# Kernel optimization log

Measured on AMD Instinct MI355X. Metric: run time of the kernel, lower is better.

## Reference

```python
import math
import jax, jax.numpy as jnp
import numpy as np

B, C, H, W = 4, 256, 64, 64
N_HEAD = 4
GROUPS = 32
EPS = 1e-5


def setup_inputs() -> dict:
    key = jax.random.key(0)
    k1, k2, k3 = jax.random.split(key, 3)
    fan = C  # 1x1 conv fan_in
    bound_qkv = math.sqrt(3.0 * 1.0 / ((fan + 3 * C) / 2))
    x = jax.random.normal(k1, (B, C, H, W), dtype=jnp.float32)
    w_qkv = jax.random.uniform(k2, (3 * C, C), dtype=jnp.float32, minval=-bound_qkv, maxval=bound_qkv)
    # out conv has scale=1e-10 init, but use small random weights for a non-trivial baseline
    w_out = jax.random.normal(k3, (C, C), dtype=jnp.float32) * 0.02
    return {
        "x": x,
        "gn_gamma": jnp.ones((C,), jnp.float32),
        "gn_beta": jnp.zeros((C,), jnp.float32),
        "w_qkv": w_qkv,
        "b_qkv": jnp.zeros((3 * C,), jnp.float32),
        "w_out": w_out,
        "b_out": jnp.zeros((C,), jnp.float32),
    }


def _group_norm(x, gamma, beta):
    b, c, h, w = x.shape
    xr = x.reshape(b, GROUPS, c // GROUPS, h, w)
    mean = xr.mean(axis=(2, 3, 4), keepdims=True)
    var = xr.var(axis=(2, 3, 4), keepdims=True)
    xn = ((xr - mean) * jax.lax.rsqrt(var + EPS)).reshape(b, c, h, w)
    return xn * gamma[None, :, None, None] + beta[None, :, None, None]


def reference(x, gn_gamma, gn_beta, w_qkv, b_qkv, w_out, b_out):
    b, c, h, w = x.shape
    head_dim = c // N_HEAD
    norm = _group_norm(x, gn_gamma, gn_beta)
    # 1x1 conv == channel matmul
    qkv = jnp.einsum('oc,bchw->bohw', w_qkv, norm) + b_qkv[None, :, None, None]
    qkv = qkv.reshape(b, N_HEAD, 3 * head_dim, h, w)
    q, k, v = jnp.split(qkv, 3, axis=2)  # each [b, n, d, h, w]
    # note: original scales by sqrt(channel), NOT sqrt(head_dim)
    attn = jnp.einsum('bnchw,bncyx->bnhwyx', q, k) / math.sqrt(c)
    attn = jax.nn.softmax(attn.reshape(b, N_HEAD, h, w, h * w), axis=-1)
    attn = attn.reshape(b, N_HEAD, h, w, h, w)
    out = jnp.einsum('bnhwyx,bncyx->bnchw', attn, v).reshape(b, c, h, w)
    out = jnp.einsum('oc,bchw->bohw', w_out, out) + b_out[None, :, None, None]
    return (out + x) / np.sqrt(2.0).astype(np.float32)
```

## Files before the change

kernel.cpp:

```cpp
#include <hip/hip_runtime.h>
#include <hip/hip_bf16.h>

#define B_   4
#define C_   256
#define HW_  4096
#define GR_  32
#define CPG_ 8
#define EPS_ 1e-5f
#define QSCALE_ 0.09016844005555897f
#define RSQRT2_ 0.70710678118654752f

typedef short bf16x8 __attribute__((ext_vector_type(8)));
typedef short bf16x4 __attribute__((ext_vector_type(4)));
typedef float f32x4  __attribute__((ext_vector_type(4)));
typedef unsigned short u16x4 __attribute__((ext_vector_type(4)));
typedef unsigned int u32x4 __attribute__((ext_vector_type(4)));

__device__ __forceinline__ unsigned short f2bf(float f) {
  unsigned int x; __builtin_memcpy(&x, &f, 4);
  x = x + 0x7FFFu + ((x >> 16) & 1u);
  return (unsigned short)(x >> 16);
}
__device__ __forceinline__ unsigned int cvtpk(float lo, float hi) {
  unsigned int r;
  asm("v_cvt_pk_bf16_f32 %0, %1, %2" : "=v"(r) : "v"(lo), "v"(hi));
  return r;
}
__device__ __forceinline__ float exp2v(float x) {
  float r;
  asm("v_exp_f32 %0, %1" : "=v"(r) : "v"(x));
  return r;
}

#define GP(p) ((const __attribute__((address_space(1))) void*)(p))
#define LP(p) ((__attribute__((address_space(3))) void*)(p))

__global__ __launch_bounds__(256) void wcvt(const float* __restrict__ wqkv,
                                            const float* __restrict__ bqkv,
                                            const float* __restrict__ wout,
                                            unsigned short* __restrict__ wbf,
                                            float* __restrict__ bias_s) {
  int i = blockIdx.x * 256 + threadIdx.x;
  const int NQ = 768 * 256, NO = 256 * 256;
  if (i < NQ) {
    int o = i >> 8;
    float s = ((o % 192) < 64) ? QSCALE_ : 1.0f;
    wbf[i] = f2bf(wqkv[i] * s);
  } else if (i < NQ + NO) {
    wbf[i] = f2bf(wout[i - NQ]);
  } else if (i < NQ + NO + 768) {
    int o = i - NQ - NO;
    float s = ((o % 192) < 64) ? QSCALE_ : 1.0f;
    bias_s[o] = bqkv[o] * s;
  }
}

__global__ __launch_bounds__(256) void gn_stats(const float* __restrict__ x,
                                                float* __restrict__ stats) {
  int bg = blockIdx.x;
  const float4* p = (const float4*)(x + (size_t)bg * (CPG_ * HW_));
  float s = 0.f, ss = 0.f;
  for (int i = threadIdx.x; i < (CPG_ * HW_ / 4); i += 256) {
    float4 v = p[i];
    s  += v.x + v.y + v.z + v.w;
    ss += v.x * v.x + v.y * v.y + v.z * v.z + v.w * v.w;
  }
  #pragma unroll
  for (int off = 32; off > 0; off >>= 1) {
    s  += __shfl_down(s, off, 64);
    ss += __shfl_down(ss, off, 64);
  }
  __shared__ float rs[4], rss[4];
  int wv = threadIdx.x >> 6;
  if ((threadIdx.x & 63) == 0) { rs[wv] = s; rss[wv] = ss; }
  __syncthreads();
  if (threadIdx.x == 0) {
    float S = rs[0] + rs[1] + rs[2] + rs[3];
    float SS = rss[0] + rss[1] + rss[2] + rss[3];
    float mean = S * (1.f / (CPG_ * HW_));
    float var = SS * (1.f / (CPG_ * HW_)) - mean * mean;
    stats[bg * 2 + 0] = mean;
    stats[bg * 2 + 1] = rsqrtf(var + EPS_);
  }
}

__global__ __launch_bounds__(512) void gemm_qkv(const unsigned short* __restrict__ wbf,
                                                const float* __restrict__ bias_s,
                                                const float* __restrict__ x,
                                                const float* __restrict__ stats,
                                                const float* __restrict__ gamma,
                                                const float* __restrict__ beta,
                                                unsigned short* __restrict__ qt,
                                                unsigned short* __restrict__ ktb,
                                                unsigned short* __restrict__ vb) {
  int p0 = blockIdx.x * 64;
  int b  = blockIdx.y;
  int lane = threadIdx.x & 63, wv = threadIdx.x >> 6;
  int cl = lane & 15, g = lane >> 4;

  __shared__ unsigned short bt[64 * 256];
  __shared__ unsigned short scratch[64][68];

  {
    int t = threadIdx.x;
    int cl16 = t & 15;
    int row32 = t >> 4;
    const float* xb = x + (size_t)b * C_ * HW_;
    #pragma unroll
    for (int cc = 0; cc < 4; ++cc) {
      int c0 = cc * 64;
      #pragma unroll
      for (int i = 0; i < 2; ++i) {
        int cloc = i * 32 + row32;
        int c = c0 + cloc;
        int bg = b * GR_ + (c >> 3);
        float mean = stats[bg * 2], rstd = stats[bg * 2 + 1];
        float a = rstd * gamma[c];
        float bb = beta[c] - mean * a;
        float4 v = *(const float4*)&xb[(size_t)c * HW_ + p0 + cl16 * 4];
        u16x4 o;
        o[0] = f2bf(v.x * a + bb); o[1] = f2bf(v.y * a + bb);
        o[2] = f2bf(v.z * a + bb); o[3] = f2bf(v.w * a + bb);
        *(u16x4*)&scratch[cloc][cl16 * 4] = o;
      }
      __syncthreads();
      #pragma unroll
      for (int i = 0; i < 2; ++i) {
        int pp = i * 32 + row32;
        u16x4 o;
        #pragma unroll
        for (int k = 0; k < 4; ++k) o[k] = scratch[cl16 * 4 + k][pp];
        int cbyte = (c0 + cl16 * 4) * 2;
        int sw = (((cbyte >> 4) ^ (pp & 7)) << 4) | (cbyte & 15);
        *(u16x4*)((char*)bt + pp * 512 + sw) = o;
      }
      __syncthreads();
    }
  }

  f32x4 z = {0.f, 0.f, 0.f, 0.f};
  f32x4 acc[6][4];
  #pragma unroll
  for (int j = 0; j < 6; ++j)
    #pragma unroll
    for (int nt = 0; nt < 4; ++nt) acc[j][nt] = z;

  const char* btc = (const char*)bt;
  for (int kc = 0; kc < C_; kc += 32) {
    bf16x8 bfr[4];
    #pragma unroll
    for (int nt = 0; nt < 4; ++nt) {
      int row = nt * 16 + cl;
      bfr[nt] = *(const bf16x8*)(btc + row * 512 + ((((kc >> 3) + g) ^ (cl & 7)) << 4));
    }
    #pragma unroll
    for (int j = 0; j < 6; ++j) {
      int rt = wv * 6 + j;
      bf16x8 af = *(const bf16x8*)&wbf[(size_t)(rt * 16 + cl) * C_ + kc + g * 8];
      #pragma unroll
      for (int nt = 0; nt < 4; ++nt)
        acc[j][nt] = __builtin_amdgcn_mfma_f32_16x16x32_bf16(af, bfr[nt], acc[j][nt], 0, 0, 0);
    }
  }

  #pragma unroll
  for (int j = 0; j < 6; ++j) {
    int rt = wv * 6 + j;
    int y = rt >> 2;
    int h = y / 3, type = y - h * 3;
    int bh = b * 4 + h;
    int olocal = (rt & 3) * 16 + g * 4;
    int obase = rt * 16 + g * 4;
    if (type == 2) {
      unsigned short* dst = vb + (size_t)bh * 64 * HW_;
      #pragma unroll
      for (int r = 0; r < 4; ++r) {
        float bv = bias_s[obase + r];
        #pragma unroll
        for (int nt = 0; nt < 4; ++nt)
          dst[(size_t)(olocal + r) * HW_ + p0 + nt * 16 + cl] = f2bf(acc[j][nt][r] + bv);
      }
    } else {
      unsigned short* dst = (type == 0 ? qt : ktb) + (size_t)bh * HW_ * 64;
      #pragma unroll
      for (int nt = 0; nt < 4; ++nt) {
        int p = p0 + nt * 16 + cl;
        u16x4 o4;
        #pragma unroll
        for (int r = 0; r < 4; ++r) o4[r] = f2bf(acc[j][nt][r] + bias_s[obase + r]);
        *(u16x4*)&dst[(size_t)p * 64 + olocal] = o4;
      }
    }
  }
}

__global__ __launch_bounds__(512) void flash_attn(const unsigned short* __restrict__ qt,
                                                  const unsigned short* __restrict__ ktb,
                                                  const unsigned short* __restrict__ vb,
                                                  unsigned short* __restrict__ attnt) {
  int bh = blockIdx.x;
  int qtile = blockIdx.y;
  int lane = threadIdx.x & 63, wv = threadIdx.x >> 6;
  int cl = lane & 15, g = lane >> 4;
  int r8 = lane >> 3;
  int gi = (lane & 7) ^ r8;

  const unsigned short* qtb = qt  + (size_t)bh * HW_ * 64;
  const unsigned short* ktp = ktb + (size_t)bh * HW_ * 64;
  const unsigned short* vbp = vb  + (size_t)bh * 64 * HW_;

  __shared__ unsigned short smem[2][8192];

  int qpix0 = qtile * 256 + wv * 32 + cl;
  bf16x8 qf0[2], qf1[2];
  qf0[0] = *(const bf16x8*)&qtb[(size_t)qpix0 * 64 + g * 8];
  qf0[1] = *(const bf16x8*)&qtb[(size_t)qpix0 * 64 + 32 + g * 8];
  qf1[0] = *(const bf16x8*)&qtb[(size_t)(qpix0 + 16) * 64 + g * 8];
  qf1[1] = *(const bf16x8*)&qtb[(size_t)(qpix0 + 16) * 64 + 32 + g * 8];

  f32x4 z = {0.f, 0.f, 0.f, 0.f};
  f32x4 oacc0[4] = {z, z, z, z};
  f32x4 oacc1[4] = {z, z, z, z};
  f32x4 lacc0 = z, lacc1 = z;

  int rdo = cl * 128 + ((g * 16) ^ ((cl & 7) << 4));
  int vbase = cl * 128 + (g & 1) * 8;
  int vxor  = (cl & 7) << 4;
  int ghalf = g >> 1;

  const unsigned short* kp = ktp + (size_t)(wv * 8 + r8) * 64 + gi * 8;
  const unsigned short* vp = vbp + (size_t)(wv * 8 + r8) * HW_ + gi * 8;

#define STAGE(bi) do {                                                              \
    unsigned short* sb = &smem[bi][0];                                              \
    __builtin_amdgcn_global_load_lds(GP(kp), LP(sb + wv * 512),        16, 0, 0);   \
    __builtin_amdgcn_global_load_lds(GP(vp), LP(sb + 4096 + wv * 512), 16, 0, 0);   \
    kp += 64 * 64;                                                                  \
    vp += 64;                                                                       \
  } while (0)

  STAGE(0);

  int cur = 0;
  for (int t = 0; t < 64; ++t) {
    if (t < 63) {
      STAGE(cur ^ 1);
      asm volatile("s_waitcnt vmcnt(2)" ::: "memory");
    } else {
      asm volatile("s_waitcnt vmcnt(0)" ::: "memory");
    }
    asm volatile("s_barrier" ::: "memory");

    const char* kb  = (const char*)&smem[cur][0];
    const char* vbx = (const char*)&smem[cur][4096];

    f32x4 sacc0[4] = {z, z, z, z};
    f32x4 sacc1[4] = {z, z, z, z};
    __builtin_amdgcn_s_setprio(1);
    #pragma unroll
    for (int nt = 0; nt < 4; ++nt) {
      #pragma unroll
      for (int ks = 0; ks < 2; ++ks) {
        bf16x8 kf = *(const bf16x8*)(kb + rdo + nt * 2048 + ks * 64);
        sacc0[nt] = __builtin_amdgcn_mfma_f32_16x16x32_bf16(kf, qf0[ks], sacc0[nt], 0, 0, 0);
        sacc1[nt] = __builtin_amdgcn_mfma_f32_16x16x32_bf16(kf, qf1[ks], sacc1[nt], 0, 0, 0);
      }
    }
    __builtin_amdgcn_s_setprio(0);

    unsigned int pk01a[4], pk23a[4], pk01b[4], pk23b[4];
    #pragma unroll
    for (int nt = 0; nt < 4; ++nt) {
      f32x4 pa, pbv;
      pa[0] = exp2v(sacc0[nt][0]); pa[1] = exp2v(sacc0[nt][1]);
      pa[2] = exp2v(sacc0[nt][2]); pa[3] = exp2v(sacc0[nt][3]);
      pbv[0] = exp2v(sacc1[nt][0]); pbv[1] = exp2v(sacc1[nt][1]);
      pbv[2] = exp2v(sacc1[nt][2]); pbv[3] = exp2v(sacc1[nt][3]);
      lacc0 += pa;
      lacc1 += pbv;
      pk01a[nt] = cvtpk(pa[0], pa[1]);
      pk23a[nt] = cvtpk(pa[2], pa[3]);
      pk01b[nt] = cvtpk(pbv[0], pbv[1]);
      pk23b[nt] = cvtpk(pbv[2], pbv[3]);
    }

    __builtin_amdgcn_s_setprio(1);
    #pragma unroll
    for (int nt = 0; nt < 4; ++nt) {
      union { unsigned int u[2]; bf16x4 v; } pb0, pb1;
      pb0.u[0] = pk01a[nt]; pb0.u[1] = pk23a[nt];
      pb1.u[0] = pk01b[nt]; pb1.u[1] = pk23b[nt];
      int gsw = ((nt * 2 + ghalf) << 4) ^ vxor;
      #pragma unroll
      for (int dt = 0; dt < 4; ++dt) {
        bf16x4 vf = *(const bf16x4*)(vbx + dt * 2048 + vbase + gsw);
        oacc0[dt] = __builtin_amdgcn_mfma_f32_16x16x16bf16_1k(vf, pb0.v, oacc0[dt], 0, 0, 0);
        oacc1[dt] = __builtin_amdgcn_mfma_f32_16x16x16bf16_1k(vf, pb1.v, oacc1[dt], 0, 0, 0);
      }
    }
    __builtin_amdgcn_s_setprio(0);
    asm volatile("s_barrier" ::: "memory");
    cur ^= 1;
  }
#undef STAGE

  float l0 = lacc0[0] + lacc0[1] + lacc0[2] + lacc0[3];
  l0 += __shfl_xor(l0, 16, 64);
  l0 += __shfl_xor(l0, 32, 64);
  float l1 = lacc1[0] + lacc1[1] + lacc1[2] + lacc1[3];
  l1 += __shfl_xor(l1, 16, 64);
  l1 += __shfl_xor(l1, 32, 64);

  int b = bh >> 2, h = bh & 3;
  float rl0 = 1.f / l0;
  float rl1 = 1.f / l1;
  unsigned short* at0 = attnt + ((size_t)b * HW_ + qpix0) * C_ + h * 64;
  unsigned short* at1 = attnt + ((size_t)b * HW_ + qpix0 + 16) * C_ + h * 64;
  #pragma unroll
  for (int dt = 0; dt < 4; ++dt) {
    u16x4 o4a, o4b;
    #pragma unroll
    for (int r = 0; r < 4; ++r) {
      o4a[r] = f2bf(oacc0[dt][r] * rl0);
      o4b[r] = f2bf(oacc1[dt][r] * rl1);
    }
    *(u16x4*)&at0[dt * 16 + g * 4] = o4a;
    *(u16x4*)&at1[dt * 16 + g * 4] = o4b;
  }
}

__global__ __launch_bounds__(512) void gemm_out(const unsigned short* __restrict__ wbf_out,
                                                const float* __restrict__ bias,
                                                const unsigned short* __restrict__ attnt,
                                                const float* __restrict__ x,
                                                float* __restrict__ out) {
  int p0 = blockIdx.x * 64;
  int b  = blockIdx.y;
  int lane = threadIdx.x & 63, wv = threadIdx.x >> 6;
  int cl = lane & 15, g = lane >> 4;

  __shared__ unsigned short bt[64 * 256];

  {
    const unsigned short* ab = attnt + ((size_t)b * HW_ + p0) * C_;
    int rowl = lane >> 5;
    int grl  = lane & 31;
    #pragma unroll
    for (int i = 0; i < 4; ++i) {
      int row = wv * 8 + i * 2 + rowl;
      int sgr = grl ^ (row & 7);
      __builtin_amdgcn_global_load_lds(GP(ab + (size_t)row * C_ + sgr * 8),
                                       LP(bt + (wv * 8 + i * 2) * C_), 16, 0, 0);
    }
  }
  __syncthreads();

  f32x4 z = {0.f, 0.f, 0.f, 0.f};
  f32x4 acc[2][4];
  #pragma unroll
  for (int j = 0; j < 2; ++j)
    #pragma unroll
    for (int nt = 0; nt < 4; ++nt) acc[j][nt] = z;

  const char* btc = (const char*)bt;
  for (int kc = 0; kc < C_; kc += 32) {
    bf16x8 bfr[4];
    #pragma unroll
    for (int nt = 0; nt < 4; ++nt) {
      int row = nt * 16 + cl;
      bfr[nt] = *(const bf16x8*)(btc + row * 512 + ((((kc >> 3) + g) ^ (cl & 7)) << 4));
    }
    #pragma unroll
    for (int j = 0; j < 2; ++j) {
      int rt = wv * 2 + j;
      bf16x8 af = *(const bf16x8*)&wbf_out[(size_t)(rt * 16 + cl) * C_ + kc + g * 8];
      #pragma unroll
      for (int nt = 0; nt < 4; ++nt)
        acc[j][nt] = __builtin_amdgcn_mfma_f32_16x16x32_bf16(af, bfr[nt], acc[j][nt], 0, 0, 0);
    }
  }

  const float* xb = x + (size_t)b * C_ * HW_;
  float* ob = out + (size_t)b * C_ * HW_;
  #pragma unroll
  for (int j = 0; j < 2; ++j) {
    int rt = wv * 2 + j;
    #pragma unroll
    for (int r = 0; r < 4; ++r) {
      int o = rt * 16 + g * 4 + r;
      float bv = bias[o];
      #pragma unroll
      for (int nt = 0; nt < 4; ++nt) {
        int p = p0 + nt * 16 + cl;
        size_t idx = (size_t)o * HW_ + p;
        ob[idx] = (acc[j][nt][r] + bv + xb[idx]) * RSQRT2_;
      }
    }
  }
}

extern "C" void kernel_launch(void* const* d_in, const int* in_sizes, int n_in,
                              void* d_out, int out_size, void* d_ws, size_t ws_size,
                              hipStream_t stream) {
  const float* x     = (const float*)d_in[0];
  const float* gamma = (const float*)d_in[1];
  const float* beta  = (const float*)d_in[2];
  const float* w_qkv = (const float*)d_in[3];
  const float* b_qkv = (const float*)d_in[4];
  const float* w_out = (const float*)d_in[5];
  const float* b_out = (const float*)d_in[6];
  float* out = (float*)d_out;

  char* ws = (char*)d_ws;
  float* stats           = (float*)ws;
  float* bias_s          = (float*)(ws + 1024);
  unsigned short* wbf    = (unsigned short*)(ws + 4096);
  unsigned short* attnt  = (unsigned short*)(ws + 528384);
  unsigned short* qt     = (unsigned short*)(ws + 8916992);
  unsigned short* ktb    = (unsigned short*)(ws + 17305600);
  unsigned short* vb     = (unsigned short*)(ws + 25694208);

  wcvt<<<dim3(1028), dim3(256), 0, stream>>>(w_qkv, b_qkv, w_out, wbf, bias_s);
  gn_stats<<<dim3(128), dim3(256), 0, stream>>>(x, stats);
  gemm_qkv<<<dim3(64, 4), dim3(512), 0, stream>>>(wbf, bias_s, x, stats, gamma, beta, qt, ktb, vb);
  flash_attn<<<dim3(16, 16), dim3(512), 0, stream>>>(qt, ktb, vb, attnt);
  gemm_out<<<dim3(64, 4), dim3(512), 0, stream>>>(wbf + 768 * 256, b_out, attnt, x, out);
}
```

Before: 145.5 us.

## Software-pipeline flash attention with triple-buffered LDS and skewed QK/PV stages

Moves the flash-attention inner loop from double to triple buffering in LDS and skews the pipeline. Each iteration now issues the QK^T MFMAs for tile t together with the PV MFMAs for tile t-1, then computes exp2 and the bf16 packing for tile t after the barrier. The aim is to interleave the transcendental softmax work with the matrix work and to keep loads two tiles ahead. The cost is 50% more shared memory per block (48KB), which may reduce occupancy, plus added prologue and epilogue code and more live registers.

Result: slower. 150.9 us (+3.7%).

```diff
diff --git a/kernel.cpp b/kernel.cpp
--- a/kernel.cpp
+++ b/kernel.cpp
@@ -209,7 +209,7 @@
   const unsigned short* ktp = ktb + (size_t)bh * HW_ * 64;
   const unsigned short* vbp = vb  + (size_t)bh * 64 * HW_;
 
-  __shared__ unsigned short smem[2][8192];
+  __shared__ unsigned short smem[3][8192];
 
   int qpix0 = qtile * 256 + wv * 32 + cl;
   bf16x8 qf0[2], qf1[2];
@@ -231,78 +231,106 @@
   const unsigned short* kp = ktp + (size_t)(wv * 8 + r8) * 64 + gi * 8;
   const unsigned short* vp = vbp + (size_t)(wv * 8 + r8) * HW_ + gi * 8;
 
-#define STAGE(bi) do {                                                              \
-    unsigned short* sb = &smem[bi][0];                                              \
-    __builtin_amdgcn_global_load_lds(GP(kp), LP(sb + wv * 512),        16, 0, 0);   \
-    __builtin_amdgcn_global_load_lds(GP(vp), LP(sb + 4096 + wv * 512), 16, 0, 0);   \
-    kp += 64 * 64;                                                                  \
-    vp += 64;                                                                       \
+  char* bA = (char*)&smem[0][0];
+  char* bB = (char*)&smem[1][0];
+  char* bC = (char*)&smem[2][0];
+
+#define STAGE(basep) do {                                                             \
+    __builtin_amdgcn_global_load_lds(GP(kp), LP((basep) + wv * 1024),        16, 0, 0); \
+    __builtin_amdgcn_global_load_lds(GP(vp), LP((basep) + 8192 + wv * 1024), 16, 0, 0); \
+    kp += 64 * 64;                                                                    \
+    vp += 64;                                                                         \
   } while (0)
 
-  STAGE(0);
-
-  int cur = 0;
-  for (int t = 0; t < 64; ++t) {
+#define QK_BLOCK(kb)                                                                  \
+    _Pragma("unroll")                                                                 \
+    for (int nt = 0; nt < 4; ++nt) {                                                  \
+      _Pragma("unroll")                                                               \
+      for (int ks = 0; ks < 2; ++ks) {                                                \
+        bf16x8 kf = *(const bf16x8*)((kb) + rdo + nt * 2048 + ks * 64);               \
+        sacc0[nt] = __builtin_amdgcn_mfma_f32_16x16x32_bf16(kf, qf0[ks], sacc0[nt], 0, 0, 0); \
+        sacc1[nt] = __builtin_amdgcn_mfma_f32_16x16x32_bf16(kf, qf1[ks], sacc1[nt], 0, 0, 0); \
+      }                                                                               \
+    }
+
+#define PV_BLOCK(vbx)                                                                 \
+    _Pragma("unroll")                                                                 \
+    for (int nt = 0; nt < 4; ++nt) {                                                  \
+      union { unsigned int u[2]; bf16x4 v; } pb0, pb1;                                \
+      pb0.u[0] = pk01a[nt]; pb0.u[1] = pk23a[nt];                                     \
+      pb1.u[0] = pk01b[nt]; pb1.u[1] = pk23b[nt];                                     \
+      int gsw = ((nt * 2 + ghalf) << 4) ^ vxor;                                       \
+      _Pragma("unroll")                                                               \
+      for (int dt = 0; dt < 4; ++dt) {                                                \
+        bf16x4 vf = *(const bf16x4*)((vbx) + dt * 2048 + vbase + gsw);                \
+        oacc0[dt] = __builtin_amdgcn_mfma_f32_16x16x16bf16_1k(vf, pb0.v, oacc0[dt], 0, 0, 0); \
+        oacc1[dt] = __builtin_amdgcn_mfma_f32_16x16x16bf16_1k(vf, pb1.v, oacc1[dt], 0, 0, 0); \
+      }                                                                               \
+    }
+
+#define SOFTMAX_BLOCK                                                                 \
+    _Pragma("unroll")                                                                 \
+    for (int nt = 0; nt < 4; ++nt) {                                                  \
+      f32x4 pa, pbv;                                                                  \
+      pa[0] = exp2v(sacc0[nt][0]); pa[1] = exp2v(sacc0[nt][1]);                       \
+      pa[2] = exp2v(sacc0[nt][2]); pa[3] = exp2v(sacc0[nt][3]);                       \
+      pbv[0] = exp2v(sacc1[nt][0]); pbv[1] = exp2v(sacc1[nt][1]);                     \
+      pbv[2] = exp2v(sacc1[nt][2]); pbv[3] = exp2v(sacc1[nt][3]);                     \
+      lacc0 += pa;                                                                    \
+      lacc1 += pbv;                                                                   \
+      pk01a[nt] = cvtpk(pa[0], pa[1]);                                                \
+      pk23a[nt] = cvtpk(pa[2], pa[3]);                                                \
+      pk01b[nt] = cvtpk(pbv[0], pbv[1]);                                              \
+      pk23b[nt] = cvtpk(pbv[2], pbv[3]);                                              \
+    }
+
+  STAGE(bA);
+  STAGE(bB);
+
+  unsigned int pk01a[4], pk23a[4], pk01b[4], pk23b[4];
+
+  asm volatile("s_waitcnt vmcnt(2)" ::: "memory");
+  asm volatile("s_barrier" ::: "memory");
+  {
+    f32x4 sacc0[4] = {z, z, z, z};
+    f32x4 sacc1[4] = {z, z, z, z};
+    __builtin_amdgcn_s_setprio(1);
+    QK_BLOCK(bA)
+    __builtin_amdgcn_s_setprio(0);
+    asm volatile("s_barrier" ::: "memory");
+    STAGE(bC);
+    SOFTMAX_BLOCK
+  }
+  { char* tmp = bA; bA = bB; bB = bC; bC = tmp; }
+
+  for (int t = 1; t < 64; ++t) {
     if (t < 63) {
-      STAGE(cur ^ 1);
       asm volatile("s_waitcnt vmcnt(2)" ::: "memory");
     } else {
       asm volatile("s_waitcnt vmcnt(0)" ::: "memory");
     }
     asm volatile("s_barrier" ::: "memory");
 
-    const char* kb  = (const char*)&smem[cur][0];
-    const char* vbx = (const char*)&smem[cur][4096];
-
     f32x4 sacc0[4] = {z, z, z, z};
     f32x4 sacc1[4] = {z, z, z, z};
     __builtin_amdgcn_s_setprio(1);
-    #pragma unroll
-    for (int nt = 0; nt < 4; ++nt) {
-      #pragma unroll
-      for (int ks = 0; ks < 2; ++ks) {
-        bf16x8 kf = *(const bf16x8*)(kb + rdo + nt * 2048 + ks * 64);
-        sacc0[nt] = __builtin_amdgcn_mfma_f32_16x16x32_bf16(kf, qf0[ks], sacc0[nt], 0, 0, 0);
-        sacc1[nt] = __builtin_amdgcn_mfma_f32_16x16x32_bf16(kf, qf1[ks], sacc1[nt], 0, 0, 0);
-      }
-    }
-    __builtin_amdgcn_s_setprio(0);
-
-    unsigned int pk01a[4], pk23a[4], pk01b[4], pk23b[4];
-    #pragma unroll
-    for (int nt = 0; nt < 4; ++nt) {
-      f32x4 pa, pbv;
-      pa[0] = exp2v(sacc0[nt][0]); pa[1] = exp2v(sacc0[nt][1]);
-      pa[2] = exp2v(sacc0[nt][2]); pa[3] = exp2v(sacc0[nt][3]);
-      pbv[0] = exp2v(sacc1[nt][0]); pbv[1] = exp2v(sacc1[nt][1]);
-      pbv[2] = exp2v(sacc1[nt][2]); pbv[3] = exp2v(sacc1[nt][3]);
-      lacc0 += pa;
-      lacc1 += pbv;
-      pk01a[nt] = cvtpk(pa[0], pa[1]);
-      pk23a[nt] = cvtpk(pa[2], pa[3]);
-      pk01b[nt] = cvtpk(pbv[0], pbv[1]);
-      pk23b[nt] = cvtpk(pbv[2], pbv[3]);
-    }
-
-    __builtin_amdgcn_s_setprio(1);
-    #pragma unroll
-    for (int nt = 0; nt < 4; ++nt) {
-      union { unsigned int u[2]; bf16x4 v; } pb0, pb1;
-      pb0.u[0] = pk01a[nt]; pb0.u[1] = pk23a[nt];
-      pb1.u[0] = pk01b[nt]; pb1.u[1] = pk23b[nt];
-      int gsw = ((nt * 2 + ghalf) << 4) ^ vxor;
-      #pragma unroll
-      for (int dt = 0; dt < 4; ++dt) {
-        bf16x4 vf = *(const bf16x4*)(vbx + dt * 2048 + vbase + gsw);
-        oacc0[dt] = __builtin_amdgcn_mfma_f32_16x16x16bf16_1k(vf, pb0.v, oacc0[dt], 0, 0, 0);
-        oacc1[dt] = __builtin_amdgcn_mfma_f32_16x16x16bf16_1k(vf, pb1.v, oacc1[dt], 0, 0, 0);
-      }
-    }
+    QK_BLOCK(bA)
+    PV_BLOCK(bC + 8192)
     __builtin_amdgcn_s_setprio(0);
     asm volatile("s_barrier" ::: "memory");
-    cur ^= 1;
-  }
+    if (t <= 61) STAGE(bC);
+    SOFTMAX_BLOCK
+    char* tmp = bA; bA = bB; bB = bC; bC = tmp;
+  }
+
+  __builtin_amdgcn_s_setprio(1);
+  PV_BLOCK(bC + 8192)
+  __builtin_amdgcn_s_setprio(0);
+
 #undef STAGE
+#undef QK_BLOCK
+#undef PV_BLOCK
+#undef SOFTMAX_BLOCK
 
   float l0 = lacc0[0] + lacc0[1] + lacc0[2] + lacc0[3];
   l0 += __shfl_xor(l0, 16, 64);
```
